# Performance work log

Hardware: AMD Instinct MI355X
Metric: run time of the kernel (lower is better)

Reference implementation:

```python
import jax, jax.numpy as jnp
import numpy as np

B, C, D, H, EXP = 4, 1024, 1024, 16, 4
EPS = 1e-6


def ffn_layernorm(x, w, b):
    # normalize over channel axis (dim 1); w,b have shape (1, C)
    u = jnp.mean(x, axis=1, keepdims=True)
    s = jnp.mean((x - u) ** 2, axis=1, keepdims=True)
    xn = (x - u) / jnp.sqrt(s + EPS)
    return w[:, :, None] * xn + b[:, :, None]


def softmax_one(x):
    # exp(x - max) / (1 + sum exp(x - max)), exactly as the torch SoftmaxOne
    m = jnp.max(x, axis=-1, keepdims=True)
    e = jnp.exp(x - m)
    return e / (1.0 + jnp.sum(e, axis=-1, keepdims=True))


def setup_inputs() -> dict:
    key = jax.random.key(0)
    ks = jax.random.split(key, 20)
    n = lambda k, shape, s=0.02: jax.random.normal(k, shape, dtype=jnp.float32) * s
    inp = {
        "x1": jax.random.normal(ks[0], (B, C, D), dtype=jnp.float32),
        "lnq_w": jnp.ones((1, C), jnp.float32) + n(ks[1], (1, C)),
        "lnq_b": n(ks[2], (1, C)),
        "lnk_w": jnp.ones((1, C), jnp.float32) + n(ks[3], (1, C)),
        "lnk_b": n(ks[4], (1, C)),
        "lnv_w": jnp.ones((1, C), jnp.float32) + n(ks[5], (1, C)),
        "lnv_b": n(ks[6], (1, C)),
        "wq": n(ks[7], (D, D)),
        "bq": n(ks[8], (D,)),
        "wk": n(ks[9], (D, D)),
        "bk": n(ks[10], (D,)),
        "wv": n(ks[11], (D, D)),
        "bv": n(ks[12], (D,)),
        "ffnln_w": jnp.ones((1, C), jnp.float32) + n(ks[13], (1, C)),
        "ffnln_b": n(ks[14], (1, C)),
        "conv1_w": n(ks[15], (C * EXP, C)),
        "conv1_b": n(ks[16], (C * EXP,)),
        "conv2_w": n(ks[17], (C, C * EXP)),
        "conv2_b": n(ks[18], (C,)),
    }
    return inp


def reference(x1, lnq_w, lnq_b, lnk_w, lnk_b, lnv_w, lnv_b,
              wq, bq, wk, bk, wv, bv,
              ffnln_w, ffnln_b, conv1_w, conv1_b, conv2_w, conv2_b):
    b, c, d = x1.shape
    dh = d // H
    q = ffn_layernorm(x1, lnq_w, lnq_b)
    k = ffn_layernorm(x1, lnk_w, lnk_b)
    v = ffn_layernorm(x1, lnv_w, lnv_b)
    # nn.Linear: y = x @ W.T + b, then the torch code's direct reshape
    # (b, c, d) -> (b, H, c, dh) (NOT a transpose-split)
    q = (q @ wq.T + bq).reshape(b, H, c, dh)
    k = (k @ wk.T + bk).reshape(b, H, c, dh)
    v = (v @ wv.T + bv).reshape(b, H, c, dh)
    scale = 1.0 / np.sqrt(dh).astype(np.float32)
    attn = jnp.einsum("bhqe,bhke->bhqk", q * scale, k)
    attn_weights = softmax_one(attn)
    o = jnp.einsum("bhqk,bhke->bhqe", attn_weights, v)
    o = o.transpose(0, 2, 1, 3).reshape(b, c, d)
    x = x1 + o
    # FFN: channel LayerNorm -> 1x1 conv (channel mix) -> GELU -> 1x1 conv
    xl = ffn_layernorm(x, ffnln_w, ffnln_b)
    h1 = jnp.einsum("oc,bcl->bol", conv1_w, xl) + conv1_b[None, :, None]
    h1 = jax.nn.gelu(h1, approximate=False)
    h2 = jnp.einsum("oc,bcl->bol", conv2_w, h1) + conv2_b[None, :, None]
    return (x + h2, attn_weights)
```

## Files before the change

kernel.cpp:

```cpp
#include <hip/hip_runtime.h>
#include <hip/hip_bf16.h>
#include <math.h>


typedef __bf16 bf16;
typedef __bf16 bf16x4 __attribute__((ext_vector_type(4)));
typedef __bf16 bf16x8 __attribute__((ext_vector_type(8)));
typedef float floatx4 __attribute__((ext_vector_type(4)));

#define MFMA16(a, b, c) __builtin_amdgcn_mfma_f32_16x16x32_bf16(a, b, c, 0, 0, 0)

__device__ __forceinline__ void gload16(const void* g, void* l) {
    __builtin_amdgcn_global_load_lds((__attribute__((address_space(1))) void*)g,
                                     (__attribute__((address_space(3))) void*)l,
                                     16, 0, 0);
}

__global__ __launch_bounds__(256)
void cast_all(const float* __restrict__ s0, bf16* __restrict__ d0_,
              const float* __restrict__ s1, bf16* __restrict__ d1_,
              const float* __restrict__ s2, bf16* __restrict__ d2_,
              const float* __restrict__ s3, bf16* __restrict__ d3_,
              const float* __restrict__ s4, bf16* __restrict__ d4_)
{
    int blk = blockIdx.x;
    const float* s; bf16* d; int base;
    if (blk < 1024)      { s = s0; d = d0_; base = blk; }
    else if (blk < 2048) { s = s1; d = d1_; base = blk - 1024; }
    else if (blk < 3072) { s = s2; d = d2_; base = blk - 2048; }
    else if (blk < 7168) { s = s3; d = d3_; base = blk - 3072; }
    else                 { s = s4; d = d4_; base = blk - 7168; }
    long i = ((long)base << 10) + (threadIdx.x << 2);
    float4 v = *(const float4*)(s + i);
    bf16x4 o;
    o[0] = (bf16)v.x; o[1] = (bf16)v.y; o[2] = (bf16)v.z; o[3] = (bf16)v.w;
    *(bf16x4*)(d + i) = o;
}

__global__ __launch_bounds__(256)
void stats_part(const float* __restrict__ xin, float* __restrict__ ps,
                float* __restrict__ pq)
{
    __shared__ float S1[4][64];
    __shared__ float S2[4][64];
    const int b = blockIdx.z, chunk = blockIdx.y;
    const int d0 = blockIdx.x << 6;
    const int tid = threadIdx.x;
    const int dl = tid & 63, cg = tid >> 6;
    const float* xp = xin + ((long)b << 20) + d0 + dl;
    const int cbase = (chunk << 8) + (cg << 6);
    float s = 0.f, sq = 0.f;
    for (int c = 0; c < 64; ++c) {
        float v = xp[(long)(cbase + c) << 10];
        s += v; sq += v * v;
    }
    S1[cg][dl] = s; S2[cg][dl] = sq;
    __syncthreads();
    if (tid < 64) {
        float ts = S1[0][tid] + S1[1][tid] + S1[2][tid] + S1[3][tid];
        float tq = S2[0][tid] + S2[1][tid] + S2[2][tid] + S2[3][tid];
        int idx = ((b * 4 + chunk) << 10) + d0 + tid;
        ps[idx] = ts; pq[idx] = tq;
    }
}

__global__ __launch_bounds__(256)
void stats_fin(const float* __restrict__ ps, const float* __restrict__ pq,
               float* __restrict__ u, float* __restrict__ rstd)
{
    int i = (blockIdx.x << 8) + threadIdx.x;
    int b = i >> 10, d = i & 1023;
    int base = (b << 12) + d;
    float s = ps[base] + ps[base + 1024] + ps[base + 2048] + ps[base + 3072];
    float q = pq[base] + pq[base + 1024] + pq[base + 2048] + pq[base + 3072];
    float mu = s * (1.f / 1024.f);
    float var = q * (1.f / 1024.f) - mu * mu;
    u[i] = mu;
    rstd[i] = rsqrtf(var + 1e-6f);
}

__global__ __launch_bounds__(256)
void ln_qkv_kernel(const float* __restrict__ x1, const float* __restrict__ u,
                   const float* __restrict__ rs,
                   const float* __restrict__ wq, const float* __restrict__ bq,
                   const float* __restrict__ wk, const float* __restrict__ bk,
                   const float* __restrict__ wv, const float* __restrict__ bv,
                   bf16* __restrict__ lnq, bf16* __restrict__ lnk,
                   bf16* __restrict__ lnv)
{
    const int bc = blockIdx.x;
    const int c = bc & 1023, b = bc >> 10;
    const int d = threadIdx.x << 2;
    const long i = ((long)bc << 10) + d;
    const float4 xv = *(const float4*)(x1 + i);
    const float4 uv = *(const float4*)(u + (b << 10) + d);
    const float4 rv = *(const float4*)(rs + (b << 10) + d);
    float xn0 = (xv.x - uv.x) * rv.x;
    float xn1 = (xv.y - uv.y) * rv.y;
    float xn2 = (xv.z - uv.z) * rv.z;
    float xn3 = (xv.w - uv.w) * rv.w;
    float sw, sb; bf16x4 o;
    sw = wq[c]; sb = bq[c];
    o[0]=(bf16)(sw*xn0+sb); o[1]=(bf16)(sw*xn1+sb); o[2]=(bf16)(sw*xn2+sb); o[3]=(bf16)(sw*xn3+sb);
    *(bf16x4*)(lnq + i) = o;
    sw = wk[c]; sb = bk[c];
    o[0]=(bf16)(sw*xn0+sb); o[1]=(bf16)(sw*xn1+sb); o[2]=(bf16)(sw*xn2+sb); o[3]=(bf16)(sw*xn3+sb);
    *(bf16x4*)(lnk + i) = o;
    sw = wv[c]; sb = bv[c];
    o[0]=(bf16)(sw*xn0+sb); o[1]=(bf16)(sw*xn1+sb); o[2]=(bf16)(sw*xn2+sb); o[3]=(bf16)(sw*xn3+sb);
    *(bf16x4*)(lnv + i) = o;
}

template<int MODE>
__global__ __launch_bounds__(256, 2)
void gemm_nt(const bf16* __restrict__ Ab, const bf16* __restrict__ Bb,
             void* __restrict__ Outb, float* __restrict__ Part,
             const float* __restrict__ bias0, const float* __restrict__ bias1,
             const float* __restrict__ bias2, const float* __restrict__ residb,
             long sAz, long sBz, long sOz, long sRz, long sPz,
             int M, int N, int K, int Ksub, int zdiv)
{
    __shared__ __align__(16) bf16 As[2][128 * 64];
    __shared__ __align__(16) bf16 Bs[2][128 * 64];
    const int z = blockIdx.z;
    const int zb = z / zdiv, kz = z % zdiv;
    const bf16* A = Ab + (long)zb * sAz + (long)kz * Ksub;
    const bf16* B = Bb + (long)zb * sBz + (long)kz * Ksub;
    const float* bias = (zb == 0) ? bias0 : (zb == 1 ? bias1 : bias2);
    const int m0 = blockIdx.y << 7, n0 = blockIdx.x << 7;
    const int tid = threadIdx.x;
    const int wave = tid >> 6, lane = tid & 63;
    const int wm = (wave & 1) << 6, wn = (wave >> 1) << 6;
    const int lm = lane & 15, quad = lane >> 4;
    const int swz = (lm & 7) << 3;
    const bf16* Ag = A + (long)m0 * K;
    const bf16* Bg = B + (long)n0 * K;

    floatx4 acc[4][4] = {};
    const int nt = Ksub >> 6;

#pragma unroll
    for (int r_ = 0; r_ < 4; ++r_) {
        int s_ = (r_ << 8) + tid;
        int lrow = s_ >> 3;
        long go = (long)lrow * K + (((s_ & 7) ^ (lrow & 7)) << 3);
        gload16(Ag + go, &As[0][s_ << 3]);
        gload16(Bg + go, &Bs[0][s_ << 3]);
    }
    __syncthreads();

    for (int t = 0; t < nt; ++t) {
        const int cur = t & 1;
        if (t + 1 < nt) {
            const int kofs = (t + 1) << 6;
#pragma unroll
            for (int r_ = 0; r_ < 4; ++r_) {
                int s_ = (r_ << 8) + tid;
                int lrow = s_ >> 3;
                long go = (long)lrow * K + kofs + (((s_ & 7) ^ (lrow & 7)) << 3);
                gload16(Ag + go, &As[cur ^ 1][s_ << 3]);
                gload16(Bg + go, &Bs[cur ^ 1][s_ << 3]);
            }
        }
        bf16x8 af[4][2], bfv[4][2];
#pragma unroll
        for (int i = 0; i < 4; ++i) {
            int rA = (wm + i * 16 + lm) << 6;
            int rB = (wn + i * 16 + lm) << 6;
#pragma unroll
            for (int ks = 0; ks < 2; ++ks) {
                int co = (ks << 5) + (quad << 3);
                af[i][ks]  = *(const bf16x8*)(&As[cur][(rA + co) ^ swz]);
                bfv[i][ks] = *(const bf16x8*)(&Bs[cur][(rB + co) ^ swz]);
            }
        }
        __builtin_amdgcn_s_setprio(1);
#pragma unroll
        for (int ks = 0; ks < 2; ++ks)
#pragma unroll
            for (int mi = 0; mi < 4; ++mi)
#pragma unroll
                for (int ni = 0; ni < 4; ++ni)
                    acc[mi][ni] = MFMA16(af[mi][ks], bfv[ni][ks], acc[mi][ni]);
        __builtin_amdgcn_s_setprio(0);
        __syncthreads();
    }

    const int quad4 = quad << 2;
    if (MODE == 2) {
        if (kz == 0) {
            float* Out = (float*)Outb + (long)zb * sOz;
            const float* R = residb + (long)zb * sRz;
#pragma unroll
            for (int mi = 0; mi < 4; ++mi)
#pragma unroll
                for (int ni = 0; ni < 4; ++ni)
#pragma unroll
                    for (int r = 0; r < 4; ++r) {
                        int row = m0 + wm + mi * 16 + quad4 + r;
                        int col = n0 + wn + ni * 16 + lm;
                        long idx = (long)row * N + col;
                        Out[idx] = acc[mi][ni][r] + bias[row] + R[idx];
                    }
        } else {
            float* Out = Part + (long)zb * sPz;
#pragma unroll
            for (int mi = 0; mi < 4; ++mi)
#pragma unroll
                for (int ni = 0; ni < 4; ++ni)
#pragma unroll
                    for (int r = 0; r < 4; ++r) {
                        int row = m0 + wm + mi * 16 + quad4 + r;
                        int col = n0 + wn + ni * 16 + lm;
                        Out[(long)row * N + col] = acc[mi][ni][r];
                    }
        }
    } else {
        bf16* Out = (bf16*)Outb + (long)zb * sOz;
#pragma unroll
        for (int mi = 0; mi < 4; ++mi)
#pragma unroll
            for (int ni = 0; ni < 4; ++ni)
#pragma unroll
                for (int r = 0; r < 4; ++r) {
                    int row = m0 + wm + mi * 16 + quad4 + r;
                    int col = n0 + wn + ni * 16 + lm;
                    float v = acc[mi][ni][r] + bias[col];
                    if (MODE == 1)
                        v = 0.5f * v * (1.0f + erff(v * 0.70710678118654752f));
                    Out[(long)row * N + col] = (bf16)v;
                }
    }
}

__global__ __launch_bounds__(256)
void addpart(float* __restrict__ out, const float* __restrict__ part)
{
    long i = (((long)blockIdx.x << 8) + threadIdx.x) << 2;
    float4 o = *(const float4*)(out + i);
    float4 p = *(const float4*)(part + i);
    o.x += p.x; o.y += p.y; o.z += p.z; o.w += p.w;
    *(float4*)(out + i) = o;
}

__global__ __launch_bounds__(256)
void vtrans_kernel(const bf16* __restrict__ v, bf16* __restrict__ vt)
{
    __shared__ bf16 T[64][66];
    const int p = blockIdx.y;
    const int k0 = blockIdx.x << 6;
    const bf16* V = v + ((long)p << 16);
    bf16* Vt = vt + ((long)p << 16);
    const int tid = threadIdx.x;
    const int e = tid & 63, g = tid >> 6;
#pragma unroll
    for (int j = 0; j < 16; ++j) {
        int kk = (g << 4) + j;
        T[e][kk] = V[((long)(k0 + kk) << 6) + e];
    }
    __syncthreads();
#pragma unroll
    for (int j = 0; j < 16; ++j) {
        int er = (g << 4) + j;
        Vt[((long)er << 10) + k0 + e] = T[er][e];
    }
}

__global__ __launch_bounds__(256)
void attn_kernel(const bf16* __restrict__ q, const bf16* __restrict__ k,
                 const bf16* __restrict__ vt, const float* __restrict__ x1,
                 float* __restrict__ attw, float* __restrict__ x)
{
    __shared__ __align__(16) bf16 Wl[16][1032];
    __shared__ float red[16][4];
    const int bid = blockIdx.x;
    const int p = ((bid & 7) << 3) | ((bid >> 3) & 7);
    const int s = bid >> 6;
    const int b = p >> 4, h = p & 15;
    const bf16* Qp = q + ((long)b << 20) + ((long)h << 16);
    const bf16* Kp = k + ((long)b << 20) + ((long)h << 16);
    const bf16* Vt = vt + ((long)p << 16);
    const int tid = threadIdx.x, w = tid >> 6, lane = tid & 63;
    const int lm = lane & 15, quad = lane >> 4;
    const int r0 = s << 4, kc0 = w << 8;

    floatx4 acc[16];
#pragma unroll
    for (int t = 0; t < 16; ++t) acc[t] = (floatx4){0.f, 0.f, 0.f, 0.f};

#pragma unroll
    for (int e0 = 0; e0 < 64; e0 += 32) {
        bf16x8 aq = *(const bf16x8*)(Qp + ((long)(r0 + lm) << 6) + e0 + quad * 8);
#pragma unroll
        for (int t = 0; t < 16; ++t) {
            bf16x8 bk = *(const bf16x8*)(Kp + ((long)(kc0 + t * 16 + lm) << 6) + e0 + quad * 8);
            acc[t] = MFMA16(aq, bk, acc[t]);
        }
    }
#pragma unroll
    for (int t = 0; t < 16; ++t)
#pragma unroll
        for (int r = 0; r < 4; ++r) acc[t][r] *= 0.125f;

    float mloc[4];
#pragma unroll
    for (int r = 0; r < 4; ++r) {
        float mm = acc[0][r];
#pragma unroll
        for (int t = 1; t < 16; ++t) mm = fmaxf(mm, acc[t][r]);
        mloc[r] = mm;
    }
#pragma unroll
    for (int off = 1; off < 16; off <<= 1)
#pragma unroll
        for (int r = 0; r < 4; ++r) mloc[r] = fmaxf(mloc[r], __shfl_xor(mloc[r], off, 64));
    if (lm == 0)
#pragma unroll
        for (int r = 0; r < 4; ++r) red[quad * 4 + r][w] = mloc[r];
    __syncthreads();
    float mfin[4];
#pragma unroll
    for (int r = 0; r < 4; ++r) {
        int row = quad * 4 + r;
        mfin[r] = fmaxf(fmaxf(red[row][0], red[row][1]), fmaxf(red[row][2], red[row][3]));
    }
    float sloc[4] = {0.f, 0.f, 0.f, 0.f};
#pragma unroll
    for (int t = 0; t < 16; ++t)
#pragma unroll
        for (int r = 0; r < 4; ++r) {
            float e = __expf(acc[t][r] - mfin[r]);
            acc[t][r] = e;
            sloc[r] += e;
        }
#pragma unroll
    for (int off = 1; off < 16; off <<= 1)
#pragma unroll
        for (int r = 0; r < 4; ++r) sloc[r] += __shfl_xor(sloc[r], off, 64);
    __syncthreads();
    if (lm == 0)
#pragma unroll
        for (int r = 0; r < 4; ++r) red[quad * 4 + r][w] = sloc[r];
    __syncthreads();
    float inv[4];
#pragma unroll
    for (int r = 0; r < 4; ++r) {
        int row = quad * 4 + r;
        inv[r] = 1.f / (1.f + red[row][0] + red[row][1] + red[row][2] + red[row][3]);
    }
#pragma unroll
    for (int r = 0; r < 4; ++r) {
        int row = quad * 4 + r;
        float iv = inv[r];
#pragma unroll
        for (int t = 0; t < 16; ++t)
            Wl[row][kc0 + t * 16 + lm] = (bf16)(acc[t][r] * iv);
    }
    __syncthreads();

    floatx4 opv[4];
#pragma unroll
    for (int ni = 0; ni < 4; ++ni) opv[ni] = (floatx4){0.f, 0.f, 0.f, 0.f};
#pragma unroll
    for (int i = 0; i < 8; ++i) {
        const int kk = kc0 + i * 32;
        bf16x8 a0 = *(const bf16x8*)&Wl[lm][kk + quad * 8];
#pragma unroll
        for (int ni = 0; ni < 4; ++ni) {
            bf16x8 bv = *(const bf16x8*)(Vt + ((long)(ni * 16 + lm) << 10) + kk + quad * 8);
            opv[ni] = MFMA16(a0, bv, opv[ni]);
        }
    }
    {
        float* attp = attw + ((long)p << 20) + ((long)r0 << 10);
#pragma unroll
        for (int i = 0; i < 16; ++i) {
            int v4 = (i << 8) + tid;
            int row = v4 >> 8, col = (v4 & 255) << 2;
            bf16x4 wv = *(const bf16x4*)&Wl[row][col];
            floatx4 o = {(float)wv[0], (float)wv[1], (float)wv[2], (float)wv[3]};
            __builtin_nontemporal_store(o, (floatx4*)(attp + ((long)row << 10) + col));
        }
    }
    __syncthreads();
    float* Ored = (float*)&Wl[0][0];
#pragma unroll
    for (int ni = 0; ni < 4; ++ni)
#pragma unroll
        for (int r = 0; r < 4; ++r)
            Ored[(w * 16 + quad * 4 + r) * 64 + ni * 16 + lm] = opv[ni][r];
    __syncthreads();
    const float* x1p = x1 + ((long)b << 20) + ((long)r0 << 10) + (h << 6);
    float* xp = x + ((long)b << 20) + ((long)r0 << 10) + (h << 6);
#pragma unroll
    for (int j = 0; j < 4; ++j) {
        int el = tid + (j << 8);
        int row = el >> 6, cc = el & 63;
        float o = Ored[row * 64 + cc] + Ored[(16 + row) * 64 + cc]
                + Ored[(32 + row) * 64 + cc] + Ored[(48 + row) * 64 + cc];
        xp[((long)row << 10) + cc] = x1p[((long)row << 10) + cc] + o;
    }
}

__global__ __launch_bounds__(256)
void ln_ffn_t_kernel(const float* __restrict__ x, const float* __restrict__ u2,
                     const float* __restrict__ r2, const float* __restrict__ fw,
                     const float* __restrict__ fb, bf16* __restrict__ xlT)
{
    __shared__ bf16 T[64][66];
    const int b = blockIdx.z;
    const int l0 = blockIdx.x << 6, c0 = blockIdx.y << 6;
    const int tid = threadIdx.x;
    const int ll = tid & 63, g = tid >> 6;
    const float uu = u2[(b << 10) + l0 + ll];
    const float rr = r2[(b << 10) + l0 + ll];
#pragma unroll
    for (int j = 0; j < 16; ++j) {
        int cc = (g << 4) + j;
        float v = x[((long)b << 20) + ((long)(c0 + cc) << 10) + l0 + ll];
        T[ll][cc] = (bf16)(fw[c0 + cc] * (v - uu) * rr + fb[c0 + cc]);
    }
    __syncthreads();
#pragma unroll
    for (int j = 0; j < 16; ++j) {
        int lr = (g << 4) + j;
        xlT[((long)b << 20) + ((long)(l0 + lr) << 10) + c0 + ll] = T[lr][ll];
    }
}

extern "C" void kernel_launch(void* const* d_in, const int* in_sizes, int n_in,
                              void* d_out, int out_size, void* d_ws, size_t ws_size,
                              hipStream_t stream)
{
    const float* x1      = (const float*)d_in[0];
    const float* lnq_w   = (const float*)d_in[1];
    const float* lnq_b   = (const float*)d_in[2];
    const float* lnk_w   = (const float*)d_in[3];
    const float* lnk_b   = (const float*)d_in[4];
    const float* lnv_w   = (const float*)d_in[5];
    const float* lnv_b   = (const float*)d_in[6];
    const float* wq      = (const float*)d_in[7];
    const float* bq      = (const float*)d_in[8];
    const float* wk      = (const float*)d_in[9];
    const float* bk      = (const float*)d_in[10];
    const float* wv      = (const float*)d_in[11];
    const float* bv      = (const float*)d_in[12];
    const float* ffnln_w = (const float*)d_in[13];
    const float* ffnln_b = (const float*)d_in[14];
    const float* conv1_w = (const float*)d_in[15];
    const float* conv1_b = (const float*)d_in[16];
    const float* conv2_w = (const float*)d_in[17];
    const float* conv2_b = (const float*)d_in[18];
    (void)in_sizes; (void)n_in; (void)out_size; (void)ws_size;

    char* ws = (char*)d_ws;
    const size_t OFF_VT   = 262144;
    const size_t OFF_QKV  = OFF_VT   + 8388608;
    const size_t OFF_WQKV = OFF_QKV  + 25165824;
    const size_t OFF_W1   = OFF_WQKV + 8388608;
    const size_t OFF_X    = OFF_W1   + 8388608;
    const size_t OFF_W2   = OFF_X    + 16777216;
    float* u1    = (float*)(ws + 0);
    float* r1    = (float*)(ws + 16384);
    float* u2    = (float*)(ws + 32768);
    float* r2    = (float*)(ws + 49152);
    float* ps    = (float*)(ws + 65536);
    float* pq    = (float*)(ws + 131072);
    bf16*  vt    = (bf16*)(ws + OFF_VT);
    bf16*  qkv   = (bf16*)(ws + OFF_QKV);
    bf16*  wqkvb = (bf16*)(ws + OFF_WQKV);
    bf16*  w1b   = (bf16*)(ws + OFF_W1);
    float* x     = (float*)(ws + OFF_X);
    bf16*  w2b   = (bf16*)(ws + OFF_W2);
    bf16*  h1T   = (bf16*)(ws + OFF_VT);
    bf16*  xlT   = (bf16*)(ws + OFF_WQKV);
    float* part  = (float*)(ws + OFF_WQKV);

    float* out0 = (float*)d_out;
    float* attw = (float*)((char*)d_out + 16777216);
    bf16*  lnqkv = (bf16*)attw;

    cast_all<<<11264, 256, 0, stream>>>(wq, wqkvb, wk, wqkvb + (1 << 20),
                                        wv, wqkvb + (2 << 20), conv1_w, w1b, conv2_w, w2b);
    stats_part<<<dim3(16, 4, 4), 256, 0, stream>>>(x1, ps, pq);
    stats_fin<<<16, 256, 0, stream>>>(ps, pq, u1, r1);
    ln_qkv_kernel<<<4096, 256, 0, stream>>>(x1, u1, r1, lnq_w, lnq_b, lnk_w, lnk_b,
                                            lnv_w, lnv_b, lnqkv, lnqkv + (1L << 22),
                                            lnqkv + (2L << 22));
    gemm_nt<0><<<dim3(8, 32, 3), 256, 0, stream>>>(lnqkv, wqkvb, qkv, nullptr, bq, bk, bv,
                                                   nullptr, 1L << 22, 1L << 20, 1L << 22, 0, 0,
                                                   4096, 1024, 1024, 1024, 1);
    vtrans_kernel<<<dim3(16, 64), 256, 0, stream>>>(qkv + (2L << 22), vt);
    attn_kernel<<<4096, 256, 0, stream>>>(qkv, qkv + (1L << 22), vt, x1, attw, x);
    stats_part<<<dim3(16, 4, 4), 256, 0, stream>>>(x, ps, pq);
    stats_fin<<<16, 256, 0, stream>>>(ps, pq, u2, r2);
    ln_ffn_t_kernel<<<dim3(16, 16, 4), 256, 0, stream>>>(x, u2, r2, ffnln_w, ffnln_b, xlT);
    gemm_nt<1><<<dim3(32, 8, 4), 256, 0, stream>>>(xlT, w1b, h1T, nullptr, conv1_b, conv1_b,
                                                   conv1_b, nullptr, 1L << 20, 0, 1L << 22, 0, 0,
                                                   1024, 4096, 1024, 1024, 1);
    gemm_nt<2><<<dim3(8, 8, 8), 256, 0, stream>>>(w2b, h1T, out0, part, conv2_b, conv2_b,
                                                  conv2_b, x, 0, 1L << 22, 1L << 20, 1L << 20,
                                                  1L << 20, 1024, 1024, 4096, 2048, 2);
    addpart<<<4096, 256, 0, stream>>>(out0, part);
}
```

Measured before the change: 624.9 us.

## Fold LayerNorm stat finalization into consumers and shrink GEMM K-tile to 32

```diff
diff --git a/kernel.cpp b/kernel.cpp
--- a/kernel.cpp
+++ b/kernel.cpp
@@ -65,23 +65,8 @@
 }
 
 __global__ __launch_bounds__(256)
-void stats_fin(const float* __restrict__ ps, const float* __restrict__ pq,
-               float* __restrict__ u, float* __restrict__ rstd)
-{
-    int i = (blockIdx.x << 8) + threadIdx.x;
-    int b = i >> 10, d = i & 1023;
-    int base = (b << 12) + d;
-    float s = ps[base] + ps[base + 1024] + ps[base + 2048] + ps[base + 3072];
-    float q = pq[base] + pq[base + 1024] + pq[base + 2048] + pq[base + 3072];
-    float mu = s * (1.f / 1024.f);
-    float var = q * (1.f / 1024.f) - mu * mu;
-    u[i] = mu;
-    rstd[i] = rsqrtf(var + 1e-6f);
-}
-
-__global__ __launch_bounds__(256)
-void ln_qkv_kernel(const float* __restrict__ x1, const float* __restrict__ u,
-                   const float* __restrict__ rs,
+void ln_qkv_kernel(const float* __restrict__ x1, const float* __restrict__ ps,
+                   const float* __restrict__ pq,
                    const float* __restrict__ wq, const float* __restrict__ bq,
                    const float* __restrict__ wk, const float* __restrict__ bk,
                    const float* __restrict__ wv, const float* __restrict__ bv,
@@ -92,13 +77,28 @@
     const int c = bc & 1023, b = bc >> 10;
     const int d = threadIdx.x << 2;
     const long i = ((long)bc << 10) + d;
+    const float* pb = ps + (b << 12) + d;
+    const float* qb = pq + (b << 12) + d;
+    float s0 = 0.f, s1 = 0.f, s2 = 0.f, s3 = 0.f;
+    float q0 = 0.f, q1 = 0.f, q2 = 0.f, q3 = 0.f;
+#pragma unroll
+    for (int c4 = 0; c4 < 4; ++c4) {
+        float4 pv = *(const float4*)(pb + (c4 << 10));
+        float4 qv = *(const float4*)(qb + (c4 << 10));
+        s0 += pv.x; s1 += pv.y; s2 += pv.z; s3 += pv.w;
+        q0 += qv.x; q1 += qv.y; q2 += qv.z; q3 += qv.w;
+    }
+    const float inv1024 = 1.f / 1024.f;
+    float u0 = s0 * inv1024, u1 = s1 * inv1024, u2 = s2 * inv1024, u3 = s3 * inv1024;
+    float r0 = rsqrtf(q0 * inv1024 - u0 * u0 + 1e-6f);
+    float r1 = rsqrtf(q1 * inv1024 - u1 * u1 + 1e-6f);
+    float r2 = rsqrtf(q2 * inv1024 - u2 * u2 + 1e-6f);
+    float r3 = rsqrtf(q3 * inv1024 - u3 * u3 + 1e-6f);
     const float4 xv = *(const float4*)(x1 + i);
-    const float4 uv = *(const float4*)(u + (b << 10) + d);
-    const float4 rv = *(const float4*)(rs + (b << 10) + d);
-    float xn0 = (xv.x - uv.x) * rv.x;
-    float xn1 = (xv.y - uv.y) * rv.y;
-    float xn2 = (xv.z - uv.z) * rv.z;
-    float xn3 = (xv.w - uv.w) * rv.w;
+    float xn0 = (xv.x - u0) * r0;
+    float xn1 = (xv.y - u1) * r1;
+    float xn2 = (xv.z - u2) * r2;
+    float xn3 = (xv.w - u3) * r3;
     float sw, sb; bf16x4 o;
     sw = wq[c]; sb = bq[c];
     o[0]=(bf16)(sw*xn0+sb); o[1]=(bf16)(sw*xn1+sb); o[2]=(bf16)(sw*xn2+sb); o[3]=(bf16)(sw*xn3+sb);
@@ -112,7 +112,7 @@
 }
 
 template<int MODE>
-__global__ __launch_bounds__(256, 2)
+__global__ __launch_bounds__(256, 3)
 void gemm_nt(const bf16* __restrict__ Ab, const bf16* __restrict__ Bb,
              void* __restrict__ Outb, float* __restrict__ Part,
              const float* __restrict__ bias0, const float* __restrict__ bias1,
@@ -120,8 +120,8 @@
              long sAz, long sBz, long sOz, long sRz, long sPz,
              int M, int N, int K, int Ksub, int zdiv)
 {
-    __shared__ __align__(16) bf16 As[2][128 * 64];
-    __shared__ __align__(16) bf16 Bs[2][128 * 64];
+    __shared__ __align__(16) bf16 As[2][128 * 32];
+    __shared__ __align__(16) bf16 Bs[2][128 * 32];
     const int z = blockIdx.z;
     const int zb = z / zdiv, kz = z % zdiv;
     const bf16* A = Ab + (long)zb * sAz + (long)kz * Ksub;
@@ -132,18 +132,17 @@
     const int wave = tid >> 6, lane = tid & 63;
     const int wm = (wave & 1) << 6, wn = (wave >> 1) << 6;
     const int lm = lane & 15, quad = lane >> 4;
-    const int swz = (lm & 7) << 3;
     const bf16* Ag = A + (long)m0 * K;
     const bf16* Bg = B + (long)n0 * K;
 
     floatx4 acc[4][4] = {};
-    const int nt = Ksub >> 6;
-
-#pragma unroll
-    for (int r_ = 0; r_ < 4; ++r_) {
+    const int nt = Ksub >> 5;
+
+#pragma unroll
+    for (int r_ = 0; r_ < 2; ++r_) {
         int s_ = (r_ << 8) + tid;
-        int lrow = s_ >> 3;
-        long go = (long)lrow * K + (((s_ & 7) ^ (lrow & 7)) << 3);
+        int lrow = s_ >> 2;
+        long go = (long)lrow * K + ((s_ & 3) << 3);
         gload16(Ag + go, &As[0][s_ << 3]);
         gload16(Bg + go, &Bs[0][s_ << 3]);
     }
@@ -152,36 +151,28 @@
     for (int t = 0; t < nt; ++t) {
         const int cur = t & 1;
         if (t + 1 < nt) {
-            const int kofs = (t + 1) << 6;
-#pragma unroll
-            for (int r_ = 0; r_ < 4; ++r_) {
+            const int kofs = (t + 1) << 5;
+#pragma unroll
+            for (int r_ = 0; r_ < 2; ++r_) {
                 int s_ = (r_ << 8) + tid;
-                int lrow = s_ >> 3;
-                long go = (long)lrow * K + kofs + (((s_ & 7) ^ (lrow & 7)) << 3);
+                int lrow = s_ >> 2;
+                long go = (long)lrow * K + kofs + ((s_ & 3) << 3);
                 gload16(Ag + go, &As[cur ^ 1][s_ << 3]);
                 gload16(Bg + go, &Bs[cur ^ 1][s_ << 3]);
             }
         }
-        bf16x8 af[4][2], bfv[4][2];
+        bf16x8 af[4], bfv[4];
 #pragma unroll
         for (int i = 0; i < 4; ++i) {
-            int rA = (wm + i * 16 + lm) << 6;
-            int rB = (wn + i * 16 + lm) << 6;
-#pragma unroll
-            for (int ks = 0; ks < 2; ++ks) {
-                int co = (ks << 5) + (quad << 3);
-                af[i][ks]  = *(const bf16x8*)(&As[cur][(rA + co) ^ swz]);
-                bfv[i][ks] = *(const bf16x8*)(&Bs[cur][(rB + co) ^ swz]);
-            }
+            af[i]  = *(const bf16x8*)(&As[cur][((wm + i * 16 + lm) << 5) + (quad << 3)]);
+            bfv[i] = *(const bf16x8*)(&Bs[cur][((wn + i * 16 + lm) << 5) + (quad << 3)]);
         }
         __builtin_amdgcn_s_setprio(1);
 #pragma unroll
-        for (int ks = 0; ks < 2; ++ks)
-#pragma unroll
-            for (int mi = 0; mi < 4; ++mi)
-#pragma unroll
-                for (int ni = 0; ni < 4; ++ni)
-                    acc[mi][ni] = MFMA16(af[mi][ks], bfv[ni][ks], acc[mi][ni]);
+        for (int mi = 0; mi < 4; ++mi)
+#pragma unroll
+            for (int ni = 0; ni < 4; ++ni)
+                acc[mi][ni] = MFMA16(af[mi], bfv[ni], acc[mi][ni]);
         __builtin_amdgcn_s_setprio(0);
         __syncthreads();
     }
@@ -403,8 +394,8 @@
 }
 
 __global__ __launch_bounds__(256)
-void ln_ffn_t_kernel(const float* __restrict__ x, const float* __restrict__ u2,
-                     const float* __restrict__ r2, const float* __restrict__ fw,
+void ln_ffn_t_kernel(const float* __restrict__ x, const float* __restrict__ ps,
+                     const float* __restrict__ pq, const float* __restrict__ fw,
                      const float* __restrict__ fb, bf16* __restrict__ xlT)
 {
     __shared__ bf16 T[64][66];
@@ -412,8 +403,14 @@
     const int l0 = blockIdx.x << 6, c0 = blockIdx.y << 6;
     const int tid = threadIdx.x;
     const int ll = tid & 63, g = tid >> 6;
-    const float uu = u2[(b << 10) + l0 + ll];
-    const float rr = r2[(b << 10) + l0 + ll];
+    float s = 0.f, q = 0.f;
+#pragma unroll
+    for (int c4 = 0; c4 < 4; ++c4) {
+        s += ps[(b << 12) + (c4 << 10) + l0 + ll];
+        q += pq[(b << 12) + (c4 << 10) + l0 + ll];
+    }
+    const float uu = s * (1.f / 1024.f);
+    const float rr = rsqrtf(q * (1.f / 1024.f) - uu * uu + 1e-6f);
 #pragma unroll
     for (int j = 0; j < 16; ++j) {
         int cc = (g << 4) + j;
@@ -460,10 +457,6 @@
     const size_t OFF_W1   = OFF_WQKV + 8388608;
     const size_t OFF_X    = OFF_W1   + 8388608;
     const size_t OFF_W2   = OFF_X    + 16777216;
-    float* u1    = (float*)(ws + 0);
-    float* r1    = (float*)(ws + 16384);
-    float* u2    = (float*)(ws + 32768);
-    float* r2    = (float*)(ws + 49152);
     float* ps    = (float*)(ws + 65536);
     float* pq    = (float*)(ws + 131072);
     bf16*  vt    = (bf16*)(ws + OFF_VT);
@@ -483,8 +476,7 @@
     cast_all<<<11264, 256, 0, stream>>>(wq, wqkvb, wk, wqkvb + (1 << 20),
                                         wv, wqkvb + (2 << 20), conv1_w, w1b, conv2_w, w2b);
     stats_part<<<dim3(16, 4, 4), 256, 0, stream>>>(x1, ps, pq);
-    stats_fin<<<16, 256, 0, stream>>>(ps, pq, u1, r1);
-    ln_qkv_kernel<<<4096, 256, 0, stream>>>(x1, u1, r1, lnq_w, lnq_b, lnk_w, lnk_b,
+    ln_qkv_kernel<<<4096, 256, 0, stream>>>(x1, ps, pq, lnq_w, lnq_b, lnk_w, lnk_b,
                                             lnv_w, lnv_b, lnqkv, lnqkv + (1L << 22),
                                             lnqkv + (2L << 22));
     gemm_nt<0><<<dim3(8, 32, 3), 256, 0, stream>>>(lnqkv, wqkvb, qkv, nullptr, bq, bk, bv,
@@ -493,8 +485,7 @@
     vtrans_kernel<<<dim3(16, 64), 256, 0, stream>>>(qkv + (2L << 22), vt);
     attn_kernel<<<4096, 256, 0, stream>>>(qkv, qkv + (1L << 22), vt, x1, attw, x);
     stats_part<<<dim3(16, 4, 4), 256, 0, stream>>>(x, ps, pq);
-    stats_fin<<<16, 256, 0, stream>>>(ps, pq, u2, r2);
-    ln_ffn_t_kernel<<<dim3(16, 16, 4), 256, 0, stream>>>(x, u2, r2, ffnln_w, ffnln_b, xlT);
+    ln_ffn_t_kernel<<<dim3(16, 16, 4), 256, 0, stream>>>(x, ps, pq, ffnln_w, ffnln_b, xlT);
     gemm_nt<1><<<dim3(32, 8, 4), 256, 0, stream>>>(xlT, w1b, h1T, nullptr, conv1_b, conv1_b,
                                                    conv1_b, nullptr, 1L << 20, 0, 1L << 22, 0, 0,
                                                    1024, 4096, 1024, 1024, 1);
```

New measurement: 622.1 us. About the same (-0.4%).
